# Optimization experiments

Measured on AMD Instinct MI355X. Metric: run time of the kernel, lower is better.

The kernel has to match this reference:

```python
import jax, jax.numpy as jnp
import numpy as np

N, G, C, H, S = 16384, 100, 10, 32, 10  # batch, nb_genes, nb_chrom, hidden, signature
BN_EPS = 1e-5
SLOPE = 0.2


def setup_inputs() -> dict:
    key = jax.random.key(0)
    k = jax.random.split(key, 7)
    x = jax.random.randint(k[0], (N, G), 0, 3)                      # categorical genotype per gene
    emb = jax.random.normal(k[1], (G, 3, H), dtype=jnp.float32)      # per-gene entity embedding tables
    gene_att = jax.random.normal(k[2], (C, H), dtype=jnp.float32)    # GeneAttentionLayer attention matrix
    chrom_att = jax.random.normal(k[3], (1, H), dtype=jnp.float32)   # ChromAttentionLayer attention vector
    W = jax.random.normal(k[4], (H, S), dtype=jnp.float32) * 0.1     # linear layer weight
    b = jnp.zeros((S,), dtype=jnp.float32)                           # linear layer bias
    bn_gamma = jnp.ones((S,), dtype=jnp.float32)
    bn_beta = jnp.zeros((S,), dtype=jnp.float32)
    return {"x": x, "emb": emb, "gene_att": gene_att, "chrom_att": chrom_att,
            "W": W, "b": b, "bn_gamma": bn_gamma, "bn_beta": bn_beta}


def reference(x, emb, gene_att, chrom_att, W, b, bn_gamma, bn_beta):
    nb_genes, nb_chrom, hid = emb.shape[0], gene_att.shape[0], emb.shape[2]
    genes_per_chrom = nb_genes // nb_chrom
    # chrom composition matrix: comp[i, j] = 1 iff gene j belongs to chromosome i (contiguous blocks)
    comp = (jnp.arange(nb_genes) // genes_per_chrom == jnp.arange(nb_chrom)[:, None]).astype(emb.dtype)

    # --- entity embedding: h[n, g] = emb[g, x[n, g]]  -> (N, G, H)
    h = emb[jnp.arange(nb_genes)[None, :], x]

    # --- GeneAttentionLayer (avoids the dense (N, C, G, H) intermediate of the torch code)
    att = jnp.einsum('ch,ngh->ncg', gene_att, h) * comp[None]        # (N, C, G)
    mask = (att != 0).astype(h.dtype)                                # matches att.bool().byte()
    a = jnp.exp(jax.nn.leaky_relu(att, SLOPE)) * mask
    a = a / jnp.maximum(a.sum(axis=2, keepdims=True), 1e-10)
    chrom = jnp.einsum('ncg,ngh->nch', a, h)                         # (N, C, H) chromosome embeddings
    chrom = jax.nn.relu(chrom)                                       # dropout p=0 -> identity

    # --- ChromAttentionLayer
    catt = jnp.einsum('h,nch->nc', chrom_att[0], chrom)              # (N, C)
    ca = jnp.exp(jax.nn.leaky_relu(catt, SLOPE))
    ca = ca / ca.sum(axis=1, keepdims=True)
    g = jnp.einsum('nc,nch->nh', ca, chrom)                          # (N, H)
    g = jax.nn.relu(g)

    # --- linear + batch norm (training-mode batch statistics, biased variance as in torch BN)
    y = g @ W + b                                                    # (N, S)
    mu = y.mean(axis=0)
    var = ((y - mu) ** 2).mean(axis=0)
    return (y - mu) / jnp.sqrt(var + BN_EPS) * bn_gamma + bn_beta
```

## Files before the change

kernel.cpp:

```cpp
#include <hip/hip_runtime.h>
#include <hip/hip_fp16.h>

#define NROWS 16384
#define NG 100
#define NC 10
#define NH 32
#define NS 10
#define GPC 10
#define SLOPE 0.2f
#define BN_EPS 1e-5f

#define RPB 32
#define BLOCK_A 512
#define NB (NROWS / RPB)

template<int CTRL>
__device__ __forceinline__ float dpp_add(float v) {
    int x = __builtin_bit_cast(int, v);
    int y = __builtin_amdgcn_update_dpp(0, x, CTRL, 0xF, 0xF, true);
    return v + __builtin_bit_cast(float, y);
}
__device__ __forceinline__ float row16_allreduce(float v) {
    v = dpp_add<0x128>(v);
    v = dpp_add<0x124>(v);
    v = dpp_add<0x122>(v);
    v = dpp_add<0x121>(v);
    return v;
}

#define GATHER(c, arr)                                                     \
    _Pragma("unroll")                                                      \
    for (int gp = 0; gp < GPC; ++gp) {                                     \
        const int g_ = (c) * GPC + gp;                                     \
        const unsigned xg_ = (pk[g_ >> 4] >> ((g_ & 15) * 2)) & 3u;        \
        const int r3_ = g_ * 3 + (int)xg_;                                 \
        arr[gp] = cmbL[r3_ * 16 + o];                                      \
    }

#define COMPUTE(arr) do {                                                  \
    float e_[GPC];                                                         \
    _Pragma("unroll")                                                      \
    for (int gp = 0; gp < GPC; ++gp)                                       \
        e_[gp] = __builtin_bit_cast(float, arr[gp].y);                     \
    const float s01_ = (e_[0] + e_[1]) + (e_[2] + e_[3]);                  \
    const float s23_ = (e_[4] + e_[5]) + (e_[6] + e_[7]);                  \
    const float suma_ = (s01_ + s23_) + (e_[8] + e_[9]);                   \
    const float inv_ = 1.f / fmaxf(suma_, 1e-10f);                         \
    float2 ch_ = {0.f, 0.f};                                               \
    _Pragma("unroll")                                                      \
    for (int gp = 0; gp < GPC; ++gp) {                                     \
        float2 hf_ = __half22float2(__builtin_bit_cast(__half2, arr[gp].x));\
        ch_.x = fmaf(e_[gp], hf_.x, ch_.x);                                \
        ch_.y = fmaf(e_[gp], hf_.y, ch_.y);                                \
    }                                                                      \
    ch_.x = fmaxf(ch_.x, 0.f);    \
    ch_.y = fmaxf(ch_.y, 0.f);                                             \
    float pc_ = ch_.x * ca.x + ch_.y * ca.y;                               \
    pc_ = row16_allreduce(pc_);                      \
    pc_ *= inv_;                                           \
    const float lc_ = pc_ > 0.f ? pc_ : SLOPE * pc_;                       \
    const float ec_ = __expf(lc_);                                         \
    const float w_ = ec_ * inv_;                                           \
    num.x = fmaf(w_, ch_.x, num.x);                                        \
    num.y = fmaf(w_, ch_.y, num.y);                                        \
    den += ec_;                                                            \
} while (0)

template<bool SLOTS>
__global__ __launch_bounds__(BLOCK_A, 4) void gga_main(
    const int* __restrict__ x, const float* __restrict__ emb,
    const float* __restrict__ gene_att, const float* __restrict__ chrom_att,
    const float* __restrict__ W, const float* __restrict__ b,
    float* __restrict__ y, float* __restrict__ P)
{
    __shared__ uint2 cmbL[300 * 16];
    __shared__ float eL[300];
    __shared__ float WTL[NS * NH];
    __shared__ float bL[NS];
    __shared__ unsigned xpL[RPB * 8];
    __shared__ float sAcc[2 * NS];

    const int t = threadIdx.x;
    const int n0 = blockIdx.x * RPB;

    if (t < 300) {
        const int g = t / 3;
        const float* ga = gene_att + (g / GPC) * NH;
        const float* e = emb + t * NH;
        float s = 0.f;
#pragma unroll
        for (int k = 0; k < NH; k += 4) {
            float4 ev = *reinterpret_cast<const float4*>(e + k);
            float4 gv = *reinterpret_cast<const float4*>(ga + k);
            s = fmaf(gv.x, ev.x, s); s = fmaf(gv.y, ev.y, s);
            s = fmaf(gv.z, ev.z, s); s = fmaf(gv.w, ev.w, s);
        }
        const float lk = s > 0.f ? s : SLOPE * s;
        eL[t] = (s != 0.f) ? __expf(lk) : 0.f;
    }
    if (t < NH * NS) WTL[t] = W[(t & 31) * NS + (t >> 5)];
    if (t < NS) bL[t] = b[t];
    if (t < 2 * NS) sAcc[t] = 0.f;
    if (t < 256) {
        const int r = t >> 3, w = t & 7;
        unsigned pw = 0u;
        if (w < 7) {
            const int4* p = reinterpret_cast<const int4*>(x + (n0 + r) * NG + w * 16);
            const int nv = (w < 6) ? 4 : 1;
#pragma unroll
            for (int i = 0; i < 4; ++i) {
                if (i < nv) {
                    int4 v = p[i];
                    pw |= ((unsigned)v.x & 3u) << (i * 8 + 0);
                    pw |= ((unsigned)v.y & 3u) << (i * 8 + 2);
                    pw |= ((unsigned)v.z & 3u) << (i * 8 + 4);
                    pw |= ((unsigned)v.w & 3u) << (i * 8 + 6);
                }
            }
        }
        xpL[r * 8 + w] = pw;
    }
    __syncthreads();

#pragma unroll
    for (int i2 = 0; i2 < 10; ++i2) {
        const int i = t + i2 * BLOCK_A;
        if (i < 4800) {
            float2 hv = reinterpret_cast<const float2*>(emb)[i];
            __half2 h2 = __floats2half2_rn(hv.x, hv.y);
            uint2 en;
            en.x = __builtin_bit_cast(unsigned, h2);
            en.y = __builtin_bit_cast(unsigned, eL[i >> 4]);
            cmbL[i] = en;
        }
    }
    __syncthreads();

    const int lr = t >> 4;
    const int o = t & 15;
    const int n = n0 + lr;

    const float2 ca = reinterpret_cast<const float2*>(chrom_att)[o];

    const uint4 pa = *reinterpret_cast<const uint4*>(&xpL[lr * 8]);
    const uint4 pb = *reinterpret_cast<const uint4*>(&xpL[lr * 8 + 4]);
    const unsigned pk[8] = {pa.x, pa.y, pa.z, pa.w, pb.x, pb.y, pb.z, pb.w};

    float2 num = {0.f, 0.f};
    float den = 0.f;

    uint2 hA[GPC], hB[GPC];
    GATHER(0, hA);
#pragma unroll
    for (int c = 0; c < NC; ++c) {
        if ((c & 1) == 0) {
            if (c + 1 < NC) { GATHER(c + 1, hB); }
            COMPUTE(hA);
        } else {
            if (c + 1 < NC) { GATHER(c + 1, hA); }
            COMPUTE(hB);
        }
    }

    const float invd = 1.f / den;
    const float g0 = fmaxf(num.x * invd, 0.f);
    const float g1 = fmaxf(num.y * invd, 0.f);

    float ys[NS];
#pragma unroll
    for (int s = 0; s < NS; ++s) {
        const float2 wv = *reinterpret_cast<const float2*>(&WTL[s * NH + o * 2]);
        float p = g0 * wv.x + g1 * wv.y;
        p = row16_allreduce(p);
        ys[s] = p + bL[s];
    }

    if (o == 0) {
        float2* yp = reinterpret_cast<float2*>(y + n * NS);
#pragma unroll
        for (int s2 = 0; s2 < 5; ++s2) yp[s2] = make_float2(ys[2 * s2], ys[2 * s2 + 1]);
    }

#pragma unroll
    for (int s = 0; s < NS; ++s) {
        float v = ys[s];
        float v2 = ys[s] * ys[s];
        v = dpp_add<0x142>(v);  v2 = dpp_add<0x142>(v2);
        v = dpp_add<0x143>(v);  v2 = dpp_add<0x143>(v2);
        if ((t & 63) == 63) {
            atomicAdd(&sAcc[s], v);
            atomicAdd(&sAcc[NS + s], v2);
        }
    }
    __syncthreads();
    if (t < 2 * NS) {
        if (SLOTS) P[t * NB + blockIdx.x] = sAcc[t];
        else       atomicAdd(&P[t], sAcc[t]);
    }
}

template<bool SLOTS>
__global__ __launch_bounds__(256) void gga_bn(
    float* __restrict__ out, const float* __restrict__ P,
    const float* __restrict__ gamma, const float* __restrict__ beta)
{
    __shared__ float red[2 * NS * 8];
    __shared__ float scL[NS], shL[NS];
    const int t = threadIdx.x;

    if (SLOTS) {
        if (t < 2 * NS * 8) {
            const int k = t >> 3, c = t & 7;
            const float4* p4 = reinterpret_cast<const float4*>(P + k * NB + c * 64);
            float s = 0.f;
#pragma unroll
            for (int i = 0; i < 16; ++i) {
                float4 v = p4[i];
                s += v.x + v.y + v.z + v.w;
            }
            red[t] = s;
        }
        __syncthreads();
    }
    if (t < NS) {
        float sm, sq;
        if (SLOTS) {
            sm = 0.f; sq = 0.f;
#pragma unroll
            for (int c = 0; c < 8; ++c) {
                sm += red[t * 8 + c];
                sq += red[(NS + t) * 8 + c];
            }
        } else {
            sm = P[t]; sq = P[NS + t];
        }
        const float mu = sm * (1.f / NROWS);
        float var = sq * (1.f / NROWS) - mu * mu;
        var = fmaxf(var, 0.f);
        const float r = rsqrtf(var + BN_EPS);
        scL[t] = gamma[t] * r;
        shL[t] = beta[t] - mu * scL[t];
    }
    __syncthreads();

    const int i4 = (blockIdx.x * 256 + t) * 4;
    float4 v = *reinterpret_cast<const float4*>(out + i4);
    const int s0 = i4 % NS;
    const int s1 = (s0 + 1) % NS, s2 = (s0 + 2) % NS, s3 = (s0 + 3) % NS;
    v.x = fmaf(v.x, scL[s0], shL[s0]);
    v.y = fmaf(v.y, scL[s1], shL[s1]);
    v.z = fmaf(v.z, scL[s2], shL[s2]);
    v.w = fmaf(v.w, scL[s3], shL[s3]);
    *reinterpret_cast<float4*>(out + i4) = v;
}

extern "C" void kernel_launch(void* const* d_in, const int* in_sizes, int n_in,
                              void* d_out, int out_size, void* d_ws, size_t ws_size,
                              hipStream_t stream) {
    const int*   x         = (const int*)d_in[0];
    const float* emb       = (const float*)d_in[1];
    const float* gene_att  = (const float*)d_in[2];
    const float* chrom_att = (const float*)d_in[3];
    const float* W         = (const float*)d_in[4];
    const float* b         = (const float*)d_in[5];
    const float* bn_gamma  = (const float*)d_in[6];
    const float* bn_beta   = (const float*)d_in[7];

    float* y = (float*)d_out;
    float* P = (float*)d_ws;

    if (ws_size >= (size_t)(2 * NS * NB * sizeof(float))) {
        gga_main<true><<<NB, BLOCK_A, 0, stream>>>(
            x, emb, gene_att, chrom_att, W, b, y, P);
        gga_bn<true><<<(NROWS * NS) / (256 * 4), 256, 0, stream>>>(
            y, P, bn_gamma, bn_beta);
    } else {
        hipMemsetAsync(P, 0, 2 * NS * sizeof(float), stream);
        gga_main<false><<<NB, BLOCK_A, 0, stream>>>(
            x, emb, gene_att, chrom_att, W, b, y, P);
        gga_bn<false><<<(NROWS * NS) / (256 * 4), 256, 0, stream>>>(
            y, P, bn_gamma, bn_beta);
    }
}
```

Measured before the change: 23.29 us.

## Split each row's chromosomes across two half-warps with 1024-thread blocks

Doubles the block to 1024 threads and gives each row 32 lanes instead of 16, with each 16-lane half handling 5 of the 10 chromosomes. The halves' partial numerator and denominator are then combined with a cross-half shuffle. The genotype packing is reorganised into two 50-gene halves, and the per-chromosome FMA chain is split into two accumulators for more instruction-level parallelism. This shortens the serial dependency chain per thread, at the cost of redundant final reductions, more threads per row and a large block that may limit occupancy under the existing launch bounds.

```diff
diff --git a/kernel.cpp b/kernel.cpp
--- a/kernel.cpp
+++ b/kernel.cpp
@@ -11,7 +11,7 @@
 #define BN_EPS 1e-5f
 
 #define RPB 32
-#define BLOCK_A 512
+#define BLOCK_A 1024
 #define NB (NROWS / RPB)
 
 template<int CTRL>
@@ -28,16 +28,15 @@
     return v;
 }
 
-#define GATHER(c, arr)                                                     \
+#define GATHER(i, arr)                                                     \
     _Pragma("unroll")                                                      \
     for (int gp = 0; gp < GPC; ++gp) {                                     \
-        const int g_ = (c) * GPC + gp;                                     \
-        const unsigned xg_ = (pk[g_ >> 4] >> ((g_ & 15) * 2)) & 3u;        \
-        const int r3_ = g_ * 3 + (int)xg_;                                 \
-        arr[gp] = cmbL[r3_ * 16 + o];                                      \
-    }
-
-#define COMPUTE(arr) do {                                                  \
+        const int gl_ = (i) * GPC + gp;                                    \
+        const unsigned xg_ = (pk[gl_ >> 4] >> ((gl_ & 15) * 2)) & 3u;      \
+        arr[gp] = cmbL[cbase + gl_ * 48 + ((int)xg_ << 4)];                \
+    }
+
+#define COMPUTE(arr, num, den) do {                                        \
     float e_[GPC];                                                         \
     _Pragma("unroll")                                                      \
     for (int gp = 0; gp < GPC; ++gp)                                       \
@@ -46,17 +45,21 @@
     const float s23_ = (e_[4] + e_[5]) + (e_[6] + e_[7]);                  \
     const float suma_ = (s01_ + s23_) + (e_[8] + e_[9]);                   \
     const float inv_ = 1.f / fmaxf(suma_, 1e-10f);                         \
-    float2 ch_ = {0.f, 0.f};                                               \
+    float2 chA_ = {0.f, 0.f}, chB_ = {0.f, 0.f};                           \
     _Pragma("unroll")                                                      \
-    for (int gp = 0; gp < GPC; ++gp) {                                     \
-        float2 hf_ = __half22float2(__builtin_bit_cast(__half2, arr[gp].x));\
-        ch_.x = fmaf(e_[gp], hf_.x, ch_.x);                                \
-        ch_.y = fmaf(e_[gp], hf_.y, ch_.y);                                \
+    for (int gp = 0; gp < GPC; gp += 2) {                                  \
+        float2 h0_ = __half22float2(__builtin_bit_cast(__half2, arr[gp].x)); \
+        float2 h1_ = __half22float2(__builtin_bit_cast(__half2, arr[gp+1].x)); \
+        chA_.x = fmaf(e_[gp],   h0_.x, chA_.x);                            \
+        chA_.y = fmaf(e_[gp],   h0_.y, chA_.y);                            \
+        chB_.x = fmaf(e_[gp+1], h1_.x, chB_.x);                            \
+        chB_.y = fmaf(e_[gp+1], h1_.y, chB_.y);                            \
     }                                                                      \
+    float2 ch_ = {chA_.x + chB_.x, chA_.y + chB_.y};                       \
     ch_.x = fmaxf(ch_.x, 0.f);    \
     ch_.y = fmaxf(ch_.y, 0.f);                                             \
     float pc_ = ch_.x * ca.x + ch_.y * ca.y;                               \
-    pc_ = row16_allreduce(pc_);                      \
+    pc_ = row16_allreduce(pc_);         \
     pc_ *= inv_;                                           \
     const float lc_ = pc_ > 0.f ? pc_ : SLOPE * pc_;                       \
     const float ec_ = __expf(lc_);                                         \
@@ -77,7 +80,7 @@
     __shared__ float eL[300];
     __shared__ float WTL[NS * NH];
     __shared__ float bL[NS];
-    __shared__ unsigned xpL[RPB * 8];
+    __shared__ unsigned xpL2[RPB * 2 * 4];
     __shared__ float sAcc[2 * NS];
 
     const int t = threadIdx.x;
@@ -102,28 +105,26 @@
     if (t < NS) bL[t] = b[t];
     if (t < 2 * NS) sAcc[t] = 0.f;
     if (t < 256) {
-        const int r = t >> 3, w = t & 7;
+        const int r = t >> 3, idx = t & 7;
+        const int h = idx >> 2, j = idx & 3;
+        const int gbase = 50 * h + 16 * j;
+        const int cnt = (j < 3) ? 16 : 2;
+        const int2* p = reinterpret_cast<const int2*>(x + (n0 + r) * NG + gbase);
         unsigned pw = 0u;
-        if (w < 7) {
-            const int4* p = reinterpret_cast<const int4*>(x + (n0 + r) * NG + w * 16);
-            const int nv = (w < 6) ? 4 : 1;
-#pragma unroll
-            for (int i = 0; i < 4; ++i) {
-                if (i < nv) {
-                    int4 v = p[i];
-                    pw |= ((unsigned)v.x & 3u) << (i * 8 + 0);
-                    pw |= ((unsigned)v.y & 3u) << (i * 8 + 2);
-                    pw |= ((unsigned)v.z & 3u) << (i * 8 + 4);
-                    pw |= ((unsigned)v.w & 3u) << (i * 8 + 6);
-                }
+#pragma unroll
+        for (int k2 = 0; k2 < 8; ++k2) {
+            if (k2 * 2 < cnt) {
+                int2 v = p[k2];
+                pw |= ((unsigned)v.x & 3u) << ((k2 * 2 + 0) * 2);
+                pw |= ((unsigned)v.y & 3u) << ((k2 * 2 + 1) * 2);
             }
         }
-        xpL[r * 8 + w] = pw;
-    }
-    __syncthreads();
-
-#pragma unroll
-    for (int i2 = 0; i2 < 10; ++i2) {
+        xpL2[(r * 2 + h) * 4 + j] = pw;
+    }
+    __syncthreads();
+
+#pragma unroll
+    for (int i2 = 0; i2 < 5; ++i2) {
         const int i = t + i2 * BLOCK_A;
         if (i < 4800) {
             float2 hv = reinterpret_cast<const float2*>(emb)[i];
@@ -136,31 +137,34 @@
     }
     __syncthreads();
 
-    const int lr = t >> 4;
-    const int o = t & 15;
+    const int lr = t >> 5;
+    const int u = t & 31;
+    const int o = u & 15;
+    const int hf = u >> 4;
     const int n = n0 + lr;
 
     const float2 ca = reinterpret_cast<const float2*>(chrom_att)[o];
 
-    const uint4 pa = *reinterpret_cast<const uint4*>(&xpL[lr * 8]);
-    const uint4 pb = *reinterpret_cast<const uint4*>(&xpL[lr * 8 + 4]);
-    const unsigned pk[8] = {pa.x, pa.y, pa.z, pa.w, pb.x, pb.y, pb.z, pb.w};
+    const uint4 pk4 = *reinterpret_cast<const uint4*>(&xpL2[(lr * 2 + hf) * 4]);
+    const unsigned pk[4] = {pk4.x, pk4.y, pk4.z, pk4.w};
+    const int cbase = hf * 2400 + o;
 
     float2 num = {0.f, 0.f};
     float den = 0.f;
 
     uint2 hA[GPC], hB[GPC];
     GATHER(0, hA);
-#pragma unroll
-    for (int c = 0; c < NC; ++c) {
-        if ((c & 1) == 0) {
-            if (c + 1 < NC) { GATHER(c + 1, hB); }
-            COMPUTE(hA);
-        } else {
-            if (c + 1 < NC) { GATHER(c + 1, hA); }
-            COMPUTE(hB);
-        }
-    }
+    {
+        GATHER(1, hB); COMPUTE(hA, num, den);
+        GATHER(2, hA); COMPUTE(hB, num, den);
+        GATHER(3, hB); COMPUTE(hA, num, den);
+        GATHER(4, hA); COMPUTE(hB, num, den);
+        COMPUTE(hA, num, den);
+    }
+
+    den += __shfl_xor(den, 16);
+    num.x += __shfl_xor(num.x, 16);
+    num.y += __shfl_xor(num.y, 16);
 
     const float invd = 1.f / den;
     const float g0 = fmaxf(num.x * invd, 0.f);
@@ -175,7 +179,7 @@
         ys[s] = p + bL[s];
     }
 
-    if (o == 0) {
+    if (u == 0) {
         float2* yp = reinterpret_cast<float2*>(y + n * NS);
 #pragma unroll
         for (int s2 = 0; s2 < 5; ++s2) yp[s2] = make_float2(ys[2 * s2], ys[2 * s2 + 1]);
@@ -183,14 +187,9 @@
 
 #pragma unroll
     for (int s = 0; s < NS; ++s) {
-        float v = ys[s];
-        float v2 = ys[s] * ys[s];
-        v = dpp_add<0x142>(v);  v2 = dpp_add<0x142>(v2);
-        v = dpp_add<0x143>(v);  v2 = dpp_add<0x143>(v2);
-        if ((t & 63) == 63) {
-            atomicAdd(&sAcc[s], v);
-            atomicAdd(&sAcc[NS + s], v2);
-        }
+        float v  = dpp_add<0x143>(ys[s]);
+        float v2 = dpp_add<0x143>(ys[s] * ys[s]);
+        if ((t & 63) == 63) { atomicAdd(&sAcc[s], v); atomicAdd(&sAcc[NS + s], v2); }
     }
     __syncthreads();
     if (t < 2 * NS) {
```

After: 29.48 us. 1.27x slower.

## Process two rows per thread group with 64 rows per block

Applied to the files above, without the earlier changes.

Doubles rows per block so each 16-lane group handles two batch rows, interleaving their gathers and computes in place of the previous double-buffered single-row pipeline. This spreads the per-block setup (embedding/attention table build in LDS, W transpose) over twice as many rows and halves the number of partial-sum slots the BN kernel reduces. The gene FMA chain is split into two accumulators for more instruction-level parallelism. Occupancy hint drops from 4 to 2 blocks per CU and register pressure rises, with only 256 blocks over the device.

```diff
diff --git a/kernel.cpp b/kernel.cpp
--- a/kernel.cpp
+++ b/kernel.cpp
@@ -10,7 +10,7 @@
 #define SLOPE 0.2f
 #define BN_EPS 1e-5f
 
-#define RPB 32
+#define RPB 64
 #define BLOCK_A 512
 #define NB (NROWS / RPB)
 
@@ -27,17 +27,22 @@
     v = dpp_add<0x121>(v);
     return v;
 }
-
-#define GATHER(c, arr)                                                     \
+__device__ __forceinline__ float uniform16_wavesum_lane63(float v) {
+    v = dpp_add<0x142>(v);
+    v = dpp_add<0x143>(v);
+    return v;
+}
+
+#define GATHER(c, arr, pkv)                                                \
     _Pragma("unroll")                                                      \
     for (int gp = 0; gp < GPC; ++gp) {                                     \
         const int g_ = (c) * GPC + gp;                                     \
-        const unsigned xg_ = (pk[g_ >> 4] >> ((g_ & 15) * 2)) & 3u;        \
+        const unsigned xg_ = (pkv[g_ >> 4] >> ((g_ & 15) * 2)) & 3u;       \
         const int r3_ = g_ * 3 + (int)xg_;                                 \
         arr[gp] = cmbL[r3_ * 16 + o];                                      \
     }
 
-#define COMPUTE(arr) do {                                                  \
+#define COMPUTE(arr, num, den) do {                                        \
     float e_[GPC];                                                         \
     _Pragma("unroll")                                                      \
     for (int gp = 0; gp < GPC; ++gp)                                       \
@@ -46,17 +51,21 @@
     const float s23_ = (e_[4] + e_[5]) + (e_[6] + e_[7]);                  \
     const float suma_ = (s01_ + s23_) + (e_[8] + e_[9]);                   \
     const float inv_ = 1.f / fmaxf(suma_, 1e-10f);                         \
-    float2 ch_ = {0.f, 0.f};                                               \
+    float2 chA_ = {0.f, 0.f}, chB_ = {0.f, 0.f};                           \
     _Pragma("unroll")                                                      \
-    for (int gp = 0; gp < GPC; ++gp) {                                     \
-        float2 hf_ = __half22float2(__builtin_bit_cast(__half2, arr[gp].x));\
-        ch_.x = fmaf(e_[gp], hf_.x, ch_.x);                                \
-        ch_.y = fmaf(e_[gp], hf_.y, ch_.y);                                \
+    for (int gp = 0; gp < GPC; gp += 2) {                                  \
+        float2 h0_ = __half22float2(__builtin_bit_cast(__half2, arr[gp].x)); \
+        float2 h1_ = __half22float2(__builtin_bit_cast(__half2, arr[gp+1].x)); \
+        chA_.x = fmaf(e_[gp],   h0_.x, chA_.x);                            \
+        chA_.y = fmaf(e_[gp],   h0_.y, chA_.y);                            \
+        chB_.x = fmaf(e_[gp+1], h1_.x, chB_.x);                            \
+        chB_.y = fmaf(e_[gp+1], h1_.y, chB_.y);                            \
     }                                                                      \
+    float2 ch_ = {chA_.x + chB_.x, chA_.y + chB_.y};                       \
     ch_.x = fmaxf(ch_.x, 0.f);    \
     ch_.y = fmaxf(ch_.y, 0.f);                                             \
     float pc_ = ch_.x * ca.x + ch_.y * ca.y;                               \
-    pc_ = row16_allreduce(pc_);                      \
+    pc_ = row16_allreduce(pc_);                                            \
     pc_ *= inv_;                                           \
     const float lc_ = pc_ > 0.f ? pc_ : SLOPE * pc_;                       \
     const float ec_ = __expf(lc_);                                         \
@@ -67,7 +76,7 @@
 } while (0)
 
 template<bool SLOTS>
-__global__ __launch_bounds__(BLOCK_A, 4) void gga_main(
+__global__ __launch_bounds__(BLOCK_A, 2) void gga_main(
     const int* __restrict__ x, const float* __restrict__ emb,
     const float* __restrict__ gene_att, const float* __restrict__ chrom_att,
     const float* __restrict__ W, const float* __restrict__ b,
@@ -101,7 +110,7 @@
     if (t < NH * NS) WTL[t] = W[(t & 31) * NS + (t >> 5)];
     if (t < NS) bL[t] = b[t];
     if (t < 2 * NS) sAcc[t] = 0.f;
-    if (t < 256) {
+    {
         const int r = t >> 3, w = t & 7;
         unsigned pw = 0u;
         if (w < 7) {
@@ -142,55 +151,59 @@
 
     const float2 ca = reinterpret_cast<const float2*>(chrom_att)[o];
 
-    const uint4 pa = *reinterpret_cast<const uint4*>(&xpL[lr * 8]);
-    const uint4 pb = *reinterpret_cast<const uint4*>(&xpL[lr * 8 + 4]);
-    const unsigned pk[8] = {pa.x, pa.y, pa.z, pa.w, pb.x, pb.y, pb.z, pb.w};
-
-    float2 num = {0.f, 0.f};
-    float den = 0.f;
-
-    uint2 hA[GPC], hB[GPC];
-    GATHER(0, hA);
+    const uint4 pa0 = *reinterpret_cast<const uint4*>(&xpL[lr * 8]);
+    const uint4 pb0 = *reinterpret_cast<const uint4*>(&xpL[lr * 8 + 4]);
+    const unsigned pk0[8] = {pa0.x, pa0.y, pa0.z, pa0.w, pb0.x, pb0.y, pb0.z, pb0.w};
+    const uint4 pa1 = *reinterpret_cast<const uint4*>(&xpL[(lr + 32) * 8]);
+    const uint4 pb1 = *reinterpret_cast<const uint4*>(&xpL[(lr + 32) * 8 + 4]);
+    const unsigned pk1[8] = {pa1.x, pa1.y, pa1.z, pa1.w, pb1.x, pb1.y, pb1.z, pb1.w};
+
+    float2 num0 = {0.f, 0.f}, num1 = {0.f, 0.f};
+    float den0 = 0.f, den1 = 0.f;
+
+    uint2 a0[GPC], a1[GPC];
 #pragma unroll
     for (int c = 0; c < NC; ++c) {
-        if ((c & 1) == 0) {
-            if (c + 1 < NC) { GATHER(c + 1, hB); }
-            COMPUTE(hA);
-        } else {
-            if (c + 1 < NC) { GATHER(c + 1, hA); }
-            COMPUTE(hB);
-        }
-    }
-
-    const float invd = 1.f / den;
-    const float g0 = fmaxf(num.x * invd, 0.f);
-    const float g1 = fmaxf(num.y * invd, 0.f);
-
-    float ys[NS];
+        GATHER(c, a0, pk0);
+        GATHER(c, a1, pk1);
+        COMPUTE(a0, num0, den0);
+        COMPUTE(a1, num1, den1);
+    }
+
+    const float invd0 = 1.f / den0;
+    const float ga0 = fmaxf(num0.x * invd0, 0.f);
+    const float ga1 = fmaxf(num0.y * invd0, 0.f);
+    const float invd1 = 1.f / den1;
+    const float gb0 = fmaxf(num1.x * invd1, 0.f);
+    const float gb1 = fmaxf(num1.y * invd1, 0.f);
+
+    float ys0[NS], ys1[NS];
 #pragma unroll
     for (int s = 0; s < NS; ++s) {
         const float2 wv = *reinterpret_cast<const float2*>(&WTL[s * NH + o * 2]);
-        float p = g0 * wv.x + g1 * wv.y;
-        p = row16_allreduce(p);
-        ys[s] = p + bL[s];
+        float p0 = ga0 * wv.x + ga1 * wv.y;
+        float p1 = gb0 * wv.x + gb1 * wv.y;
+        p0 = row16_allreduce(p0);
+        p1 = row16_allreduce(p1);
+        ys0[s] = p0 + bL[s];
+        ys1[s] = p1 + bL[s];
     }
 
     if (o == 0) {
-        float2* yp = reinterpret_cast<float2*>(y + n * NS);
-#pragma unroll
-        for (int s2 = 0; s2 < 5; ++s2) yp[s2] = make_float2(ys[2 * s2], ys[2 * s2 + 1]);
+        float2* yp0 = reinterpret_cast<float2*>(y + n * NS);
+        float2* yp1 = reinterpret_cast<float2*>(y + (n + 32) * NS);
+#pragma unroll
+        for (int s2 = 0; s2 < 5; ++s2) {
+            yp0[s2] = make_float2(ys0[2 * s2], ys0[2 * s2 + 1]);
+            yp1[s2] = make_float2(ys1[2 * s2], ys1[2 * s2 + 1]);
+        }
     }
 
 #pragma unroll
     for (int s = 0; s < NS; ++s) {
-        float v = ys[s];
-        float v2 = ys[s] * ys[s];
-        v = dpp_add<0x142>(v);  v2 = dpp_add<0x142>(v2);
-        v = dpp_add<0x143>(v);  v2 = dpp_add<0x143>(v2);
-        if ((t & 63) == 63) {
-            atomicAdd(&sAcc[s], v);
-            atomicAdd(&sAcc[NS + s], v2);
-        }
+        float v  = uniform16_wavesum_lane63(ys0[s] + ys1[s]);
+        float v2 = uniform16_wavesum_lane63(ys0[s] * ys0[s] + ys1[s] * ys1[s]);
+        if ((t & 63) == 63) { atomicAdd(&sAcc[s], v); atomicAdd(&sAcc[NS + s], v2); }
     }
     __syncthreads();
     if (t < 2 * NS) {
@@ -211,10 +224,10 @@
     if (SLOTS) {
         if (t < 2 * NS * 8) {
             const int k = t >> 3, c = t & 7;
-            const float4* p4 = reinterpret_cast<const float4*>(P + k * NB + c * 64);
+            const float4* p4 = reinterpret_cast<const float4*>(P + k * NB + c * 32);
             float s = 0.f;
 #pragma unroll
-            for (int i = 0; i < 16; ++i) {
+            for (int i = 0; i < 8; ++i) {
                 float4 v = p4[i];
                 s += v.x + v.y + v.z + v.w;
             }
```

Result: slower. 44.91 us (+92.8%).
